# Kernel optimization log

Hardware: AMD Instinct MI355X
Metric: run time of the kernel (lower is better)

Reference implementation:

```python
import jax, jax.numpy as jnp
import numpy as np

PERIODS = (1, 2, 4, 8, 16, 32, 64, 128)
INPUT_DIM = 256
OUTPUT_DIM = 512
N = OUTPUT_DIM // len(PERIODS)  # 64 units per clock group


def setup_inputs() -> dict:
    key = jax.random.key(0)
    ks = jax.random.split(key, 3 + len(PERIODS))
    B, T = 64, 2048
    inp = {
        "X": jax.random.normal(ks[0], (B, T, INPUT_DIM), dtype=jnp.float32),
        "W": jax.random.normal(ks[1], (INPUT_DIM, OUTPUT_DIM), dtype=jnp.float32) * 0.05,
        "b": jnp.zeros((OUTPUT_DIM,), dtype=jnp.float32),
    }
    # clock_weights[period_i] has shape ((P - i) * n, n): group i reads from all
    for i in range(len(PERIODS)):
        inp[f"Wc{i}"] = jax.random.normal(ks[3 + i], ((len(PERIODS) - i) * N, N), dtype=jnp.float32) * 0.05
    return inp


def reference(X, W, b, Wc0, Wc1, Wc2, Wc3, Wc4, Wc5, Wc6, Wc7):
    Wcs = [Wc0, Wc1, Wc2, Wc3, Wc4, Wc5, Wc6, Wc7]
    B, T, _ = X.shape
    # One-time input projection: (B,T,D) @ (D,O) + b -> (T,B,O) for the scan.
    x = jnp.moveaxis(jnp.einsum("btd,do->bto", X, W) + b, 1, 0)

    def step(h, inp):
        t, x_t = inp  # t: scalar int, x_t: (B, O)
        parts = []
        for i, p in enumerate(PERIODS):
            # candidate update for group i: input drive + recurrence from groups i..P-1
            upd = x_t[:, i * N:(i + 1) * N] + h[:, i * N:] @ Wcs[i]
            old = h[:, i * N:(i + 1) * N]
            parts.append(jnp.where(t % p == 0, upd, old))
        h_new = jnp.tanh(jnp.concatenate(parts, axis=1))
        return h_new, None

    h0 = jnp.zeros((B, OUTPUT_DIM), dtype=X.dtype)
    h_final, _ = jax.lax.scan(step, h0, (jnp.arange(T), x))
    return h_final  # outputs[-1]: (B, OUTPUT_DIM)
```

## Files before the change

### kernel.cpp

```cpp
#include <hip/hip_runtime.h>
#include <hip/hip_fp16.h>
#include <stdint.h>
#include <type_traits>


typedef _Float16 half_t;
typedef _Float16 h2 __attribute__((ext_vector_type(2)));
typedef _Float16 h8 __attribute__((ext_vector_type(8)));
typedef float f4 __attribute__((ext_vector_type(4)));

__device__ __forceinline__ float dot2f(h2 a, h2 b, float c) {
#if defined(__has_builtin)
#if __has_builtin(__builtin_amdgcn_fdot2)
  return __builtin_amdgcn_fdot2(a, b, c, false);
#else
  return c + (float)a[0] * (float)b[0] + (float)a[1] * (float)b[1];
#endif
#else
  return c + (float)a[0] * (float)b[0] + (float)a[1] * (float)b[1];
#endif
}

__device__ __forceinline__ float fast_tanh(float x) {
#if defined(__has_builtin)
#if __has_builtin(__builtin_amdgcn_exp2f) && __has_builtin(__builtin_amdgcn_rcpf)
  float e = __builtin_amdgcn_exp2f(x * 2.885390081777927f);
  return 1.0f - 2.0f * __builtin_amdgcn_rcpf(e + 1.0f);
#else
  float e = __builtin_exp2f(x * 2.885390081777927f);
  return 1.0f - 2.0f / (e + 1.0f);
#endif
#else
  float e = exp2f(x * 2.885390081777927f);
  return 1.0f - 2.0f / (e + 1.0f);
#endif
}

__device__ __forceinline__ float u2f(unsigned short u) {
  return (float)__builtin_bit_cast(half_t, u);
}

__device__ __forceinline__ float red3(float v) {
  float a = __shfl_xor(v, 16);
  float b = __shfl_xor(v, 32);
  float d = __shfl_xor(v, 48);
  return (v + a) + (b + d);
}

__device__ __forceinline__ void wg_barrier_lds() {
  __builtin_amdgcn_sched_barrier(0);
  asm volatile("s_waitcnt lgkmcnt(0)" ::: "memory");
  __builtin_amdgcn_s_barrier();
  __builtin_amdgcn_sched_barrier(0);
}

__device__ __forceinline__ void gl_lds16(const half_t* g, half_t* l) {
  __builtin_amdgcn_global_load_lds(
      (__attribute__((address_space(1))) void*)(void*)g,
      (__attribute__((address_space(3))) void*)(void*)l, 16, 0, 0);
}

__global__ void cw_cvt_x(const float* __restrict__ X, half_t* __restrict__ Xh, long n4) {
  long i = (long)blockIdx.x * blockDim.x + threadIdx.x;
  const long stride = (long)gridDim.x * blockDim.x;
  const float4* X4 = (const float4*)X;
  h2* out2 = (h2*)Xh;
  for (; i < n4; i += stride) {
    float4 v = X4[i];
    h2 a; a[0] = (half_t)v.x; a[1] = (half_t)v.y;
    h2 b; b[0] = (half_t)v.z; b[1] = (half_t)v.w;
    out2[2 * i] = a;
    out2[2 * i + 1] = b;
  }
}

__global__ void cw_cvt_wt(const float* __restrict__ W, half_t* __restrict__ WT) {
  int idx = blockIdx.x * 256 + threadIdx.x;
  int o = idx >> 8, d = idx & 255;
  WT[idx] = (half_t)W[d * 512 + o];
}

__global__ __launch_bounds__(256) void cw_xproj(const half_t* __restrict__ Xh,
                                                const half_t* __restrict__ WT,
                                                const float* __restrict__ bias,
                                                half_t* __restrict__ xout) {
  const int mod = blockIdx.y;
  const int Ti = 2048 >> mod;
  const long Mi = (long)64 * Ti;
  const long m0r = (long)blockIdx.x * 256;
  if (m0r >= Mi) return;
  __shared__ alignas(16) half_t Bs[64 * 256];
  __shared__ alignas(16) half_t As[256 * 64];
  const int tid = threadIdx.x;
  const int wv = tid >> 6, l = tid & 63;
  const int lr = l & 15, lk = (l >> 4) * 8;
  const int shf = 11 - mod;

#pragma unroll
  for (int it = 0; it < 8; ++it) {
    int slot = it * 256 + tid;
    int n = slot >> 5, kc = slot & 31;
    gl_lds16(WT + ((mod << 6) + n) * 256 + kc * 8, Bs + slot * 8);
  }

  f4 acc[4][4];
#pragma unroll
  for (int a = 0; a < 4; ++a)
#pragma unroll
    for (int bq = 0; bq < 4; ++bq) acc[a][bq] = f4{0.f, 0.f, 0.f, 0.f};

  for (int kt = 0; kt < 4; ++kt) {
#pragma unroll
    for (int it = 0; it < 8; ++it) {
      int slot = it * 256 + tid;
      int r = slot >> 3, kc = slot & 7;
      long m = m0r + r;
      long g = (m >> shf) * 2048 + ((m & (long)(Ti - 1)) << mod);
      gl_lds16(Xh + g * 256 + kt * 64 + kc * 8, As + slot * 8);
    }
    __syncthreads();
#pragma unroll
    for (int ks = 0; ks < 2; ++ks) {
      h8 af[4], bf[4];
#pragma unroll
      for (int mi = 0; mi < 4; ++mi)
        af[mi] = *(const h8*)&As[(wv * 64 + mi * 16 + lr) * 64 + ks * 32 + lk];
#pragma unroll
      for (int ni = 0; ni < 4; ++ni)
        bf[ni] = *(const h8*)&Bs[(ni * 16 + lr) * 256 + kt * 64 + ks * 32 + lk];
#pragma unroll
      for (int mi = 0; mi < 4; ++mi)
#pragma unroll
        for (int ni = 0; ni < 4; ++ni)
          acc[mi][ni] = __builtin_amdgcn_mfma_f32_16x16x32_f16(af[mi], bf[ni], acc[mi][ni], 0, 0, 0);
    }
    __syncthreads();
  }

  const long xb = 16777216L - (16777216L >> mod);
#pragma unroll
  for (int ni = 0; ni < 4; ++ni) {
    int n = ni * 16 + lr;
    float bv = bias[(mod << 6) + n];
#pragma unroll
    for (int mi = 0; mi < 4; ++mi) {
      f4 cf = acc[mi][ni];
#pragma unroll
      for (int q = 0; q < 4; ++q) {
        long m = m0r + wv * 64 + mi * 16 + (l >> 4) * 4 + q;
        xout[xb + m * 64 + n] = (half_t)(cf[q] + bv);
      }
    }
  }
}


template <int PAIR>
__device__ __forceinline__ void scan_role(
    const unsigned short* __restrict__ xb16,
    const float* __restrict__ Wf, const float* __restrict__ Ws,
    float* __restrict__ out, half_t (*hbuf)[512], int b) {
  constexpr int P4Fv[4] = {64, 56, 48, 40};
  constexpr int HBFv[4] = {0, 32, 64, 96};
  constexpr int P4Sv[4] = {16, 24, 32, 8};
  constexpr int HBSv[4] = {192, 160, 128, 224};
  constexpr int SSHv[4] = {6, 5, 4, 7};
  constexpr long FXBv[4] = {0L, 8388608L, 12582912L, 14680064L};
  constexpr long SXBv[4] = {16515072L, 16252928L, 15728640L, 16646144L};
  constexpr int FBASEv[4] = {0, 64, 128, 192};
  constexpr int SBASEv[4] = {384, 320, 256, 448};
  constexpr int P4F = P4Fv[PAIR], HBF = HBFv[PAIR];
  constexpr int P4S = P4Sv[PAIR], HBS = HBSv[PAIR], SSH = SSHv[PAIR];
  constexpr int FB = FBASEv[PAIR], SB = SBASEv[PAIR];
  constexpr int SROWS = 2048 >> SSH;
  constexpr int SMASK = (1 << SSH) - 1;

  const int tid = threadIdx.x;
  const int wv = tid >> 6, l = tid & 63;
  const int half = wv & 1;
  const int q = l >> 4;
  const int cl = l & 15;
  const int colA = 32 * half + cl;
  const int colB = colA + 16;
  const int sg01 = q & 1;
  const bool ownFast = (l < 32);
  const int ownCol = 32 * half + 16 * sg01 + cl;

  h2 wfA[P4F], wfB[P4F], wsA[P4S], wsB[P4S];
  if constexpr (PAIR == 0) {
#pragma unroll
    for (int g = 0; g < 16; ++g) {
      const int gg = (g + 2 * q) & 15;
#pragma unroll
      for (int j = 0; j < 4; ++j) {
        int pr = (q << 6) + gg * 4 + j;
        wfA[g * 4 + j] = h2{(half_t)Wf[(2 * pr) * 64 + colA], (half_t)Wf[(2 * pr + 1) * 64 + colA]};
        wfB[g * 4 + j] = h2{(half_t)Wf[(2 * pr) * 64 + colB], (half_t)Wf[(2 * pr + 1) * 64 + colB]};
      }
    }
  } else {
#pragma unroll
    for (int p = 0; p < P4F; ++p) {
      int pr = q * P4F + p;
      wfA[p] = h2{(half_t)Wf[(2 * pr) * 64 + colA], (half_t)Wf[(2 * pr + 1) * 64 + colA]};
      wfB[p] = h2{(half_t)Wf[(2 * pr) * 64 + colB], (half_t)Wf[(2 * pr + 1) * 64 + colB]};
    }
  }
#pragma unroll
  for (int p = 0; p < P4S; ++p) {
    int pr = q * P4S + p;
    wsA[p] = h2{(half_t)Ws[(2 * pr) * 64 + colA], (half_t)Ws[(2 * pr + 1) * 64 + colA]};
    wsB[p] = h2{(half_t)Ws[(2 * pr) * 64 + colB], (half_t)Ws[(2 * pr + 1) * 64 + colB]};
  }

  hbuf[0][tid] = (half_t)0.f;
  hbuf[1][tid] = (half_t)0.f;

  const unsigned short* xp = ownFast
      ? (xb16 + FXBv[PAIR] + ((long)b << (17 - PAIR)) + ownCol)
      : (xb16 + SXBv[PAIR] + ((long)b << (17 - SSH)) + ownCol);

  unsigned short xr0 = 0, xr1 = 0, xr2 = 0, xr3 = 0, xrS = 0;
  if (ownFast) {
    xr0 = xp[0];
    if constexpr (PAIR == 0) { xr1 = xp[64]; xr2 = xp[128]; xr3 = xp[192]; }
    if constexpr (PAIR == 1) { xr1 = xp[64]; }
  } else {
    xrS = xp[0];
  }
  float hs = 0.f;
  __syncthreads();

  auto stepf = [&](auto offc, int t, const half_t* hin, half_t* hout) {
    constexpr int OFF = decltype(offc)::value;
    const h2* hin2 = (const h2*)hin;
    constexpr bool FACT = (PAIR == 0) || (PAIR == 1 && (OFF & 1) == 0) ||
                          (PAIR >= 2 && OFF == 0);
    float vA = 0.f, vB = 0.f, vSA = 0.f, vSB = 0.f;
    bool fup = false;
    if constexpr (FACT) {
      if constexpr (PAIR == 3) fup = ((t & 7) == 0);
      else fup = true;
      if (fup) {
        float a0 = 0.f, a1 = 0.f, a2 = 0.f, a3 = 0.f;
        float b0 = 0.f, b1 = 0.f, b2 = 0.f, b3 = 0.f;
        if constexpr (PAIR == 0) {
          const h2* hp = hin2 + (q << 6);
#pragma unroll
          for (int g = 0; g < 16; ++g) {
            const int gg = (g + 2 * q) & 15;
            h2 h0 = hp[gg * 4 + 0], h1 = hp[gg * 4 + 1];
            h2 h2v = hp[gg * 4 + 2], h3 = hp[gg * 4 + 3];
            a0 = dot2f(h0, wfA[g * 4 + 0], a0); b0 = dot2f(h0, wfB[g * 4 + 0], b0);
            a1 = dot2f(h1, wfA[g * 4 + 1], a1); b1 = dot2f(h1, wfB[g * 4 + 1], b1);
            a2 = dot2f(h2v, wfA[g * 4 + 2], a2); b2 = dot2f(h2v, wfB[g * 4 + 2], b2);
            a3 = dot2f(h3, wfA[g * 4 + 3], a3); b3 = dot2f(h3, wfB[g * 4 + 3], b3);
          }
        } else {
          const h2* hp = hin2 + HBF + q * P4F;
#pragma unroll
          for (int p = 0; p < P4F; p += 4) {
            h2 h0 = hp[p], h1 = hp[p + 1], h2v = hp[p + 2], h3 = hp[p + 3];
            a0 = dot2f(h0, wfA[p + 0], a0); b0 = dot2f(h0, wfB[p + 0], b0);
            a1 = dot2f(h1, wfA[p + 1], a1); b1 = dot2f(h1, wfB[p + 1], b1);
            a2 = dot2f(h2v, wfA[p + 2], a2); b2 = dot2f(h2v, wfB[p + 2], b2);
            a3 = dot2f(h3, wfA[p + 3], a3); b3 = dot2f(h3, wfB[p + 3], b3);
          }
        }
        vA = red3((a0 + a1) + (a2 + a3));
        vB = red3((b0 + b1) + (b2 + b3));
      }
    }
    bool sup = false;
    if constexpr (OFF == 0) {
      sup = ((t & SMASK) == 0);
      if (sup) {
        float a0 = 0.f, a1 = 0.f, a2 = 0.f, a3 = 0.f;
        float b0 = 0.f, b1 = 0.f, b2 = 0.f, b3 = 0.f;
        const h2* hp = hin2 + HBS + q * P4S;
#pragma unroll
        for (int p = 0; p < P4S; p += 4) {
          h2 h0 = hp[p], h1 = hp[p + 1], h2v = hp[p + 2], h3 = hp[p + 3];
          a0 = dot2f(h0, wsA[p + 0], a0); b0 = dot2f(h0, wsB[p + 0], b0);
          a1 = dot2f(h1, wsA[p + 1], a1); b1 = dot2f(h1, wsB[p + 1], b1);
          a2 = dot2f(h2v, wsA[p + 2], a2); b2 = dot2f(h2v, wsB[p + 2], b2);
          a3 = dot2f(h3, wsA[p + 3], a3); b3 = dot2f(h3, wsB[p + 3], b3);
        }
        vSA = red3((a0 + a1) + (a2 + a3));
        vSB = red3((b0 + b1) + (b2 + b3));
      }
    }
    bool myUpd = ownFast ? fup : sup;
    float mySum = ownFast ? (sg01 ? vB : vA) : (sg01 ? vSB : vSA);
    float xv;
    if (ownFast) {
      if constexpr (PAIR == 0) {
        if constexpr (OFF == 0) xv = u2f(xr0);
        else if constexpr (OFF == 1) xv = u2f(xr1);
        else if constexpr (OFF == 2) xv = u2f(xr2);
        else xv = u2f(xr3);
      } else if constexpr (PAIR == 1) {
        xv = (OFF == 0) ? u2f(xr0) : u2f(xr1);
      } else {
        xv = u2f(xr0);
      }
    } else {
      xv = u2f(xrS);
    }
    float s = myUpd ? (mySum + xv) : hs;
    hs = fast_tanh(s);
    hout[(ownFast ? FB : SB) + ownCol] = (half_t)hs;
    if (ownFast) {
      if constexpr (PAIR == 0) {
        int tn = t + OFF + 4;
        if (tn < 2048) {
          unsigned short nv = xp[(long)tn << 6];
          if constexpr (OFF == 0) xr0 = nv;
          else if constexpr (OFF == 1) xr1 = nv;
          else if constexpr (OFF == 2) xr2 = nv;
          else xr3 = nv;
        }
      } else if constexpr (PAIR == 1) {
        if constexpr (OFF == 0) {
          int rn = (t >> 1) + 2;
          if (rn < 1024) xr0 = xp[(long)rn << 6];
        } else if constexpr (OFF == 2) {
          int rn = (t >> 1) + 3;
          if (rn < 1024) xr1 = xp[(long)rn << 6];
        }
      } else if constexpr (PAIR == 2) {
        if constexpr (OFF == 0) {
          int ni = (t >> 2) + 1;
          if (ni < 512) xr0 = xp[(long)ni << 6];
        }
      } else {
        if constexpr (OFF == 0) {
          if (fup) {
            int ni = (t >> 3) + 1;
            if (ni < 256) xr0 = xp[(long)ni << 6];
          }
        }
      }
    } else {
      if (sup) {
        int ni = (t >> SSH) + 1;
        if (ni < SROWS) xrS = xp[(long)ni << 6];
      }
    }
    wg_barrier_lds();
  };

  for (int t = 0; t < 2048; t += 4) {
    stepf(std::integral_constant<int, 0>{}, t, hbuf[0], hbuf[1]);
    stepf(std::integral_constant<int, 1>{}, t, hbuf[1], hbuf[0]);
    stepf(std::integral_constant<int, 2>{}, t, hbuf[0], hbuf[1]);
    stepf(std::integral_constant<int, 3>{}, t, hbuf[1], hbuf[0]);
  }

  out[((long)b << 9) + (ownFast ? FB : SB) + ownCol] = hs;
}

__global__ __launch_bounds__(512, 1) void cw_scan12(
    const half_t* __restrict__ xbuf,
    const float* __restrict__ Wc0, const float* __restrict__ Wc1,
    const float* __restrict__ Wc2, const float* __restrict__ Wc3,
    const float* __restrict__ Wc4, const float* __restrict__ Wc5,
    const float* __restrict__ Wc6, const float* __restrict__ Wc7,
    float* __restrict__ out) {
  __shared__ alignas(16) half_t hbuf[2][512];
  const int b = blockIdx.x;
  const unsigned short* xb16 = (const unsigned short*)xbuf;
  const int pair = threadIdx.x >> 7;
  if (pair == 0) scan_role<0>(xb16, Wc0, Wc6, out, hbuf, b);
  else if (pair == 1) scan_role<1>(xb16, Wc1, Wc5, out, hbuf, b);
  else if (pair == 2) scan_role<2>(xb16, Wc2, Wc4, out, hbuf, b);
  else scan_role<3>(xb16, Wc3, Wc7, out, hbuf, b);
}

extern "C" void kernel_launch(void* const* d_in, const int* in_sizes, int n_in,
                              void* d_out, int out_size, void* d_ws, size_t ws_size,
                              hipStream_t stream) {
  const float* X = (const float*)d_in[0];
  const float* W = (const float*)d_in[1];
  const float* bias = (const float*)d_in[2];
  const float* Wc0 = (const float*)d_in[3];
  const float* Wc1 = (const float*)d_in[4];
  const float* Wc2 = (const float*)d_in[5];
  const float* Wc3 = (const float*)d_in[6];
  const float* Wc4 = (const float*)d_in[7];
  const float* Wc5 = (const float*)d_in[8];
  const float* Wc6 = (const float*)d_in[9];
  const float* Wc7 = (const float*)d_in[10];
  float* out = (float*)d_out;

  half_t* Xh = (half_t*)d_ws;
  half_t* WT = (half_t*)((char*)d_ws + 67108864);
  half_t* xbuf = (half_t*)((char*)d_ws + 67371008);

  cw_cvt_x<<<4096, 256, 0, stream>>>(X, Xh, 8388608L);
  cw_cvt_wt<<<512, 256, 0, stream>>>(W, WT);
  dim3 g(512, 8);
  cw_xproj<<<g, 256, 0, stream>>>(Xh, WT, bias, xbuf);
  cw_scan12<<<64, 512, 0, stream>>>(xbuf, Wc0, Wc1, Wc2, Wc3, Wc4, Wc5, Wc6, Wc7, out);
}
```

Measured before the change: 1.529 ms.

## Store projected inputs time-contiguous and load eight timesteps per vector read

The projection kernel now writes each (batch, unit) column of projected inputs contiguously along time, instead of laying out rows per timestep. The scan loop then reads 8 fp16 timesteps at once as two 64-bit words, keeps a double-buffered next chunk, and picks the current value by shifting. This replaces the scalar per-step global loads in the serial recurrence with one vector load every eight updates. In exchange, the projection's stores become strided along time, which may hurt write coalescing, and each scan step adds runtime select and shift logic.

New measurement: 1.416 ms. 7.3% less time.

```diff
diff --git a/kernel.cpp b/kernel.cpp
--- a/kernel.cpp
+++ b/kernel.cpp
@@ -148,12 +148,13 @@
 #pragma unroll
       for (int q = 0; q < 4; ++q) {
         long m = m0r + wv * 64 + mi * 16 + (l >> 4) * 4 + q;
-        xout[xb + m * 64 + n] = (half_t)(cf[q] + bv);
-      }
-    }
-  }
-}
-
+        long bidx = m >> shf;
+        long trow = m & (long)(Ti - 1);
+        xout[xb + (bidx * 64 + n) * (long)Ti + trow] = (half_t)(cf[q] + bv);
+      }
+    }
+  }
+}
 
 template <int PAIR>
 __device__ __forceinline__ void scan_role(
@@ -174,6 +175,8 @@
   constexpr int FB = FBASEv[PAIR], SB = SBASEv[PAIR];
   constexpr int SROWS = 2048 >> SSH;
   constexpr int SMASK = (1 << SSH) - 1;
+  constexpr int PEXPF = PAIR;
+  constexpr int TRF = 2048 >> PEXPF;
 
   const int tid = threadIdx.x;
   const int wv = tid >> 6, l = tid & 63;
@@ -216,18 +219,14 @@
   hbuf[0][tid] = (half_t)0.f;
   hbuf[1][tid] = (half_t)0.f;
 
-  const unsigned short* xp = ownFast
-      ? (xb16 + FXBv[PAIR] + ((long)b << (17 - PAIR)) + ownCol)
-      : (xb16 + SXBv[PAIR] + ((long)b << (17 - SSH)) + ownCol);
-
-  unsigned short xr0 = 0, xr1 = 0, xr2 = 0, xr3 = 0, xrS = 0;
-  if (ownFast) {
-    xr0 = xp[0];
-    if constexpr (PAIR == 0) { xr1 = xp[64]; xr2 = xp[128]; xr3 = xp[192]; }
-    if constexpr (PAIR == 1) { xr1 = xp[64]; }
-  } else {
-    xrS = xp[0];
-  }
+  constexpr int MYROWS_F = TRF, MYROWS_S = SROWS;
+  const unsigned long long* xq = (const unsigned long long*)(
+      ownFast ? (xb16 + FXBv[PAIR] + ((long)b * 64 + ownCol) * MYROWS_F)
+              : (xb16 + SXBv[PAIR] + ((long)b * 64 + ownCol) * MYROWS_S));
+  const int myRows = ownFast ? MYROWS_F : MYROWS_S;
+  unsigned long long cLo = xq[0], cHi = xq[1];
+  unsigned long long nLo = xq[2], nHi = xq[3];
+
   float hs = 0.f;
   __syncthreads();
 
@@ -292,59 +291,20 @@
     }
     bool myUpd = ownFast ? fup : sup;
     float mySum = ownFast ? (sg01 ? vB : vA) : (sg01 ? vSB : vSA);
-    float xv;
-    if (ownFast) {
-      if constexpr (PAIR == 0) {
-        if constexpr (OFF == 0) xv = u2f(xr0);
-        else if constexpr (OFF == 1) xv = u2f(xr1);
-        else if constexpr (OFF == 2) xv = u2f(xr2);
-        else xv = u2f(xr3);
-      } else if constexpr (PAIR == 1) {
-        xv = (OFF == 0) ? u2f(xr0) : u2f(xr1);
-      } else {
-        xv = u2f(xr0);
-      }
-    } else {
-      xv = u2f(xrS);
-    }
+    const int tact = t + OFF;
+    const int e = ownFast ? (tact >> PEXPF) : (t >> SSH);
+    const int k = e & 7;
+    unsigned long long w = (k & 4) ? cHi : cLo;
+    float xv = u2f((unsigned short)(w >> ((k & 3) * 16)));
     float s = myUpd ? (mySum + xv) : hs;
     hs = fast_tanh(s);
     hout[(ownFast ? FB : SB) + ownCol] = (half_t)hs;
-    if (ownFast) {
-      if constexpr (PAIR == 0) {
-        int tn = t + OFF + 4;
-        if (tn < 2048) {
-          unsigned short nv = xp[(long)tn << 6];
-          if constexpr (OFF == 0) xr0 = nv;
-          else if constexpr (OFF == 1) xr1 = nv;
-          else if constexpr (OFF == 2) xr2 = nv;
-          else xr3 = nv;
-        }
-      } else if constexpr (PAIR == 1) {
-        if constexpr (OFF == 0) {
-          int rn = (t >> 1) + 2;
-          if (rn < 1024) xr0 = xp[(long)rn << 6];
-        } else if constexpr (OFF == 2) {
-          int rn = (t >> 1) + 3;
-          if (rn < 1024) xr1 = xp[(long)rn << 6];
-        }
-      } else if constexpr (PAIR == 2) {
-        if constexpr (OFF == 0) {
-          int ni = (t >> 2) + 1;
-          if (ni < 512) xr0 = xp[(long)ni << 6];
-        }
-      } else {
-        if constexpr (OFF == 0) {
-          if (fup) {
-            int ni = (t >> 3) + 1;
-            if (ni < 256) xr0 = xp[(long)ni << 6];
-          }
-        }
-      }
-    } else {
-      if (sup) {
-        int ni = (t >> SSH) + 1;
-        if (ni < SROWS) xrS = xp[(long)ni << 6];
+    if (myUpd && k == 7) {
+      cLo = nLo; cHi = nHi;
+      int nc = (e >> 3) + 2;
+      if (nc * 8 < myRows) {
+        nLo = xq[nc * 2];
+        nHi = xq[nc * 2 + 1];
       }
     }
     wg_barrier_lds();
@@ -360,7 +320,7 @@
   out[((long)b << 9) + (ownFast ? FB : SB) + ownCol] = hs;
 }
 
-__global__ __launch_bounds__(512, 1) void cw_scan12(
+__global__ __launch_bounds__(512, 1) void cw_scan14(
     const half_t* __restrict__ xbuf,
     const float* __restrict__ Wc0, const float* __restrict__ Wc1,
     const float* __restrict__ Wc2, const float* __restrict__ Wc3,
@@ -401,5 +361,5 @@
   cw_cvt_wt<<<512, 256, 0, stream>>>(W, WT);
   dim3 g(512, 8);
   cw_xproj<<<g, 256, 0, stream>>>(Xh, WT, bias, xbuf);
-  cw_scan12<<<64, 512, 0, stream>>>(xbuf, Wc0, Wc1, Wc2, Wc3, Wc4, Wc5, Wc6, Wc7, out);
-}
+  cw_scan14<<<64, 512, 0, stream>>>(xbuf, Wc0, Wc1, Wc2, Wc3, Wc4, Wc5, Wc6, Wc7, out);
+}
```
